# Kernel optimization log

Hardware: AMD Instinct MI355X
Metric: run time of the kernel (lower is better)

The kernel has to match this reference:

```python
import jax, jax.numpy as jnp
import numpy as np
from jax import lax

B, L = 128, 256
DW, DC = 100, 30
H = 400          # hidden_size (bidirectional total)
HD = H // 2      # per-direction hidden
NT = 18          # tag vocab size (BIOES)
VW, VC = 400000, 50000


def setup_inputs():
    key = jax.random.key(0)
    ks = iter(jax.random.split(key, 64))
    rn = lambda shape, s=0.1: jax.random.normal(next(ks), shape, jnp.float32) * s
    inp = {
        "words": jax.random.randint(next(ks), (B, L), 0, VW),
        "cap_words": jax.random.randint(next(ks), (B, L), 0, VC),
        "seq_len": jax.random.randint(next(ks), (B,), L // 2, L + 1),
        "target": jax.random.randint(next(ks), (B, L), 0, NT),
        "word_emb": rn((VW, DW)),
        "char_emb": rn((VC, DC)),
    }
    for l, din in ((0, DW + DC), (1, H)):
        for d in ("f", "b"):
            inp[f"W_ih_l{l}{d}"] = rn((4 * HD, din))
            inp[f"W_hh_l{l}{d}"] = rn((4 * HD, HD))
            inp[f"b_ih_l{l}{d}"] = rn((4 * HD,))
            inp[f"b_hh_l{l}{d}"] = rn((4 * HD,))
    inp["Wf"], inp["bf"] = rn((NT, HD)), jnp.zeros((NT,), jnp.float32)
    inp["Wb"], inp["bb"] = rn((NT, HD)), jnp.zeros((NT,), jnp.float32)
    inp["trans"] = rn((NT, NT))
    return inp


def _lstm_dir(x, W_ih, W_hh, b_ih, b_hh):
    # x: [B, L, D] -> hidden states [B, L, HD]; torch gate order i, f, g, o
    Bsz = x.shape[0]
    def step(carry, xt):
        h, c = carry
        g = xt @ W_ih.T + b_ih + h @ W_hh.T + b_hh
        i, f, gg, o = jnp.split(g, 4, axis=-1)
        c = jax.nn.sigmoid(f) * c + jax.nn.sigmoid(i) * jnp.tanh(gg)
        h = jax.nn.sigmoid(o) * jnp.tanh(c)
        return (h, c), h
    init = (jnp.zeros((Bsz, HD), x.dtype), jnp.zeros((Bsz, HD), x.dtype))
    _, hs = lax.scan(step, init, jnp.swapaxes(x, 0, 1))
    return jnp.swapaxes(hs, 0, 1)


def _rev(x, seq_len):
    # reverse each sequence within its true length (padding stays in place),
    # emulating pack_padded_sequence semantics for the backward direction
    t = jnp.arange(x.shape[1])[None, :]
    idx = jnp.where(t < seq_len[:, None], seq_len[:, None] - 1 - t, t)
    return jnp.take_along_axis(x, idx[:, :, None], axis=1)


def _crf_nll(logits, tags, mask, trans):
    # normalizer: forward algorithm, logsumexp scan over time with mask
    def step(alpha, inp):
        emit, m = inp  # emit: [B, NT], m: [B] bool
        new = jax.nn.logsumexp(alpha[:, :, None] + trans[None] + emit[:, None, :], axis=1)
        return jnp.where(m[:, None], new, alpha), None
    emits = jnp.swapaxes(logits, 0, 1)  # [L, B, NT]
    ms = jnp.swapaxes(mask, 0, 1)
    alpha, _ = lax.scan(step, emits[0], (emits[1:], ms[1:]))
    z = jax.nn.logsumexp(alpha, axis=1)
    # gold path score
    mf = mask.astype(logits.dtype)
    emit_sc = jnp.take_along_axis(logits, tags[:, :, None], axis=2)[:, :, 0]
    gold = jnp.sum(emit_sc * mf, axis=1) + jnp.sum(trans[tags[:, :-1], tags[:, 1:]] * mf[:, 1:], axis=1)
    return z - gold  # per-sample negative log-likelihood, shape [B]


def _model(words, cap_words, seq_len, target, word_emb, char_emb,
           W_ih_l0f, W_hh_l0f, b_ih_l0f, b_hh_l0f, W_ih_l0b, W_hh_l0b, b_ih_l0b, b_hh_l0b,
           W_ih_l1f, W_hh_l1f, b_ih_l1f, b_hh_l1f, W_ih_l1b, W_hh_l1b, b_ih_l1b, b_hh_l1b,
           Wf, bf, Wb, bb, trans):
    mask = jnp.arange(L)[None, :] < seq_len[:, None]  # [B, L] bool
    mf = mask.astype(jnp.float32)[:, :, None]
    x = jnp.concatenate([word_emb[words], char_emb[cap_words]], axis=-1)
    layers = (((W_ih_l0f, W_hh_l0f, b_ih_l0f, b_hh_l0f), (W_ih_l0b, W_hh_l0b, b_ih_l0b, b_hh_l0b)),
              ((W_ih_l1f, W_hh_l1f, b_ih_l1f, b_hh_l1f), (W_ih_l1b, W_hh_l1b, b_ih_l1b, b_hh_l1b)))
    h = x
    for fp, bp in layers:
        fwd = _lstm_dir(h, *fp)
        bwd = _rev(_lstm_dir(_rev(h, seq_len), *bp), seq_len)
        h = jnp.concatenate([fwd, bwd], axis=-1) * mf  # zero padded steps like packed LSTM
    forwards, backwards = h[..., :HD], h[..., HD:]
    logits = forwards @ Wf.T + bf + backwards @ Wb.T + bb
    return _crf_nll(logits, target, mask, trans)


def reference(words, cap_words, seq_len, target, word_emb, char_emb,
              W_ih_l0f, W_hh_l0f, b_ih_l0f, b_hh_l0f, W_ih_l0b, W_hh_l0b, b_ih_l0b, b_hh_l0b,
              W_ih_l1f, W_hh_l1f, b_ih_l1f, b_hh_l1f, W_ih_l1b, W_hh_l1b, b_ih_l1b, b_hh_l1b,
              Wf, bf, Wb, bb, trans):
    return _model(words, cap_words, seq_len, target, word_emb, char_emb,
                  W_ih_l0f, W_hh_l0f, b_ih_l0f, b_hh_l0f, W_ih_l0b, W_hh_l0b, b_ih_l0b, b_hh_l0b,
                  W_ih_l1f, W_hh_l1f, b_ih_l1f, b_hh_l1f, W_ih_l1b, W_hh_l1b, b_ih_l1b, b_hh_l1b,
                  Wf, bf, Wb, bb, trans)
```

## Files before the change

### kernel.cpp

```cpp
#include <hip/hip_runtime.h>
#include <math.h>

#define B_   128
#define L_   256
#define DW_  100
#define DC_  30
#define HD_  200
#define NT_  18
#define SG   4
#define KP0  160
#define KP1  416

typedef _Float16 half8 __attribute__((ext_vector_type(8)));
typedef _Float16 half4 __attribute__((ext_vector_type(4)));
typedef float    f32x4 __attribute__((ext_vector_type(4)));

__device__ __forceinline__ float frcp_(float x) { return __builtin_amdgcn_rcpf(x); }
__device__ __forceinline__ float sigm_(float x) { return frcp_(1.0f + __expf(-x)); }
__device__ __forceinline__ float tanh_(float x) { return 1.0f - 2.0f * frcp_(1.0f + __expf(2.0f * x)); }

__global__ void k_embed(const int* __restrict__ words, const int* __restrict__ caps,
                        const float* __restrict__ wemb, const float* __restrict__ cemb,
                        _Float16* __restrict__ x) {
    int pos = blockIdx.x;
    int w = words[pos], c = caps[pos];
    _Float16* xp = x + (size_t)pos * KP0;
    for (int t = threadIdx.x; t < KP0; t += blockDim.x) {
        float v = 0.f;
        if (t < DW_) v = wemb[(size_t)w * DW_ + t];
        else if (t < DW_ + DC_) v = cemb[(size_t)c * DC_ + (t - DW_)];
        xp[t] = (_Float16)v;
    }
}

__global__ void k_perm_ih16(const float* __restrict__ src, _Float16* __restrict__ dst,
                            int K, int Kpad, int colOff) {
    int i = blockIdx.x * blockDim.x + threadIdx.x;
    if (i >= 800 * Kpad) return;
    int r = i / Kpad, k = i - r * Kpad;
    int jh = r % 200, g = r / 200;
    int col = colOff + (jh << 2) + g;
    dst[(size_t)col * Kpad + k] = (k < K) ? (_Float16)src[(size_t)r * K + k] : (_Float16)0.f;
}

__global__ void k_bias_perm(const float* bi_f, const float* bh_f,
                            const float* bi_b, const float* bh_b, float* bias) {
    int j = blockIdx.x * blockDim.x + threadIdx.x;
    if (j >= 1600) return;
    int dir = j / 800, r = j - dir * 800;
    int col = dir * 800 + ((r % 200) << 2) + (r / 200);
    bias[col] = dir ? (bi_b[r] + bh_b[r]) : (bi_f[r] + bh_f[r]);
}

__global__ void k_wlog(const float* __restrict__ Wf, const float* __restrict__ bfv,
                       const float* __restrict__ Wb, const float* __restrict__ bbv,
                       float* __restrict__ wlog, float* __restrict__ blog) {
    int i = blockIdx.x * blockDim.x + threadIdx.x;
    if (i < NT_ * 400) {
        int t = i / 400, k = i - t * 400;
        wlog[i] = (k < HD_) ? Wf[t * HD_ + k] : Wb[t * HD_ + (k - HD_)];
    }
    if (i < NT_) blog[i] = bfv[i] + bbv[i];
}

__global__ __launch_bounds__(256) void k_gemm16(const _Float16* __restrict__ A,
                                                const _Float16* __restrict__ Bt,
                                                const float* __restrict__ bias,
                                                _Float16* __restrict__ C,
                                                int Kpad) {
    __shared__ __align__(16) _Float16 sA[128 * 40];
    __shared__ __align__(16) _Float16 sB[64 * 40];
    const int tid = threadIdx.x;
    const int w = tid >> 6, l = tid & 63, l15 = l & 15, lq = l >> 4;
    const int m0 = blockIdx.y * 128, n0 = blockIdx.x * 64;
    const int rw = (w >> 1) * 64, cw = (w & 1) * 32;
    f32x4 acc[4][2];
    #pragma unroll
    for (int i = 0; i < 4; i++)
        #pragma unroll
        for (int j = 0; j < 2; j++) acc[i][j] = f32x4{0.f, 0.f, 0.f, 0.f};

    for (int k0 = 0; k0 < Kpad; k0 += 32) {
        {
            int m = tid >> 1, c = (tid & 1) << 4;
            const _Float16* ap = A + (size_t)(m0 + m) * Kpad + k0 + c;
            *(half8*)&sA[m * 40 + c]     = *(const half8*)ap;
            *(half8*)&sA[m * 40 + c + 8] = *(const half8*)(ap + 8);
        }
        {
            int n = tid >> 2, k8 = (tid & 3) << 3;
            *(half8*)&sB[n * 40 + k8] = *(const half8*)&Bt[(size_t)(n0 + n) * Kpad + k0 + k8];
        }
        __syncthreads();
        half8 aF[4], bF[2];
        #pragma unroll
        for (int i = 0; i < 4; i++) aF[i] = *(const half8*)&sA[(rw + i * 16 + l15) * 40 + lq * 8];
        #pragma unroll
        for (int j = 0; j < 2; j++) bF[j] = *(const half8*)&sB[(cw + j * 16 + l15) * 40 + lq * 8];
        #pragma unroll
        for (int i = 0; i < 4; i++)
            #pragma unroll
            for (int j = 0; j < 2; j++)
                acc[i][j] = __builtin_amdgcn_mfma_f32_16x16x32_f16(aF[i], bF[j], acc[i][j], 0, 0, 0);
        __syncthreads();
    }
    #pragma unroll
    for (int j = 0; j < 2; j++) {
        int n = n0 + cw + j * 16 + l15;
        float bv = bias[n];
        #pragma unroll
        for (int i = 0; i < 4; i++) {
            int mrow = m0 + rw + i * 16 + lq * 4;
            #pragma unroll
            for (int r = 0; r < 4; r++)
                C[(size_t)(mrow + r) * 1600 + n] = (_Float16)(acc[i][j][r] + bv);
        }
    }
}

__global__ __launch_bounds__(512, 2) void k_scan4(const _Float16* __restrict__ gates,
                                                  const float* __restrict__ Whh_f,
                                                  const float* __restrict__ Whh_b,
                                                  const int* __restrict__ seq_len,
                                                  _Float16* __restrict__ hout, int ldH) {
    const int dir = blockIdx.x & 1;
    const int b0  = (blockIdx.x >> 1) * SG;
    const int tid = threadIdx.x;
    const int w   = tid >> 6;
    const int l   = tid & 63;
    const int l15 = l & 15;
    const int lq  = l >> 4;

    __shared__ __align__(16) _Float16 hA[2][16 * 232];
    __shared__ __align__(16) float    gbw[8 * 476];
    __shared__ __align__(16) _Float16 bEx[2 * 7 * 512];
    __shared__ __align__(16) _Float16 glds[2][3200];
    __shared__ int ssl[SG];

    const float* W = dir ? Whh_b : Whh_f;
    const int nT = (w < 2) ? 7 : 6;

    half8 Breg[6][7];
    #pragma unroll
    for (int i = 0; i < 6; i++) {
        int n  = (w * 6 + i) * 16 + l15;
        int jh = n >> 2, g = n & 3;
        const float* Wr = W + (size_t)(g * 200 + jh) * 200;
        #pragma unroll
        for (int kt = 0; kt < 7; kt++) {
            int k0 = kt * 32 + lq * 8;
            half8 f;
            #pragma unroll
            for (int j = 0; j < 8; j++) {
                int k = k0 + j;
                f[j] = (k < 200) ? (_Float16)Wr[k] : (_Float16)0.f;
            }
            Breg[i][kt] = f;
        }
    }
    if (w < 2) {
        int n  = (48 + w) * 16 + l15;
        int jh = n >> 2, g = n & 3;
        const float* Wr = W + (size_t)(g * 200 + jh) * 200;
        for (int kt = 0; kt < 7; kt++) {
            int k0 = kt * 32 + lq * 8;
            half8 f;
            for (int j = 0; j < 8; j++) {
                int k = k0 + j;
                f[j] = (k < 200) ? (_Float16)Wr[k] : (_Float16)0.f;
            }
            *(half8*)&bEx[(w * 7 + kt) * 512 + l * 8] = f;
        }
    }
    for (int i = tid; i < 2 * 16 * 232; i += 512) (&hA[0][0])[i] = (_Float16)0.f;
    if (tid < SG) ssl[tid] = seq_len[b0 + tid];

    const int  v    = tid;
    const bool stv  = v < 400;
    const int  m_st = v / 100;
    const int  u_st = v - m_st * 100;
    const int  sl_st = stv ? seq_len[b0 + m_st] : L_;
    const _Float16* gbase_st = gates + ((size_t)(b0 + m_st) * L_) * 1600 + dir * 800 + u_st * 8;

    const int cA = l;
    const int cB = l + 64;
    const bool vB = cB < nT * 16;
    const int iA = cA >> 4,           nhA = (cA >> 2) & 3, mA = cA & 3;
    const int iB = cB >> 4,           nhB = (cB >> 2) & 3, mB = cB & 3;
    const int igA = (iA < 6) ? (w * 6 + iA) : (48 + w);
    const int igB = (iB < 6) ? (w * 6 + iB) : (48 + w);
    const int hAcol = igA * 4 + nhA;
    const int hBcol = igB * 4 + nhB;
    float csA = 0.f, csB = 0.f;

    half8 stg;
    if (stv) {
        int rn = dir ? ((sl_st > 0) ? sl_st - 1 : 0) : 0;
        stg = *(const half8*)(gbase_st + (size_t)rn * 1600);
        *(half8*)&glds[0][v * 8] = stg;
    }
    __syncthreads();

    const f32x4 Cz = {0.f, 0.f, 0.f, 0.f};
    for (int t = 0; t < L_; t++) {
        const int p = t & 1;

        half8 stgn;
        const bool doStg = stv && (t + 1 < L_);
        if (doStg) {
            int tn = t + 1;
            int rn = dir ? ((tn < sl_st) ? sl_st - 1 - tn : tn) : tn;
            stgn = *(const half8*)(gbase_st + (size_t)rn * 1600);
        }

        if (t > 0) {
            int tp = t - 1;
            #pragma unroll
            for (int kk = 0; kk < 2; kk++) {
                int idx = tid + (kk << 9);
                if (idx < 800) {
                    int b = (idx * 5243) >> 20;
                    int hh = idx - b * 200;
                    int slb = ssl[b];
                    int row = dir ? ((tp < slb) ? slb - 1 - tp : tp) : tp;
                    _Float16 val = (tp < slb) ? hA[p][b * 232 + hh] : (_Float16)0.f;
                    hout[((size_t)(b0 + b) * L_ + row) * ldH + dir * HD_ + hh] = val;
                }
            }
        }

        f32x4 C[7];
        #pragma unroll
        for (int i = 0; i < 7; i++) C[i] = Cz;
        #pragma unroll
        for (int kt = 0; kt < 7; kt++) {
            half8 aF = *(const half8*)&hA[p][l15 * 232 + kt * 32 + lq * 8];
            #pragma unroll
            for (int i = 0; i < 6; i++)
                C[i] = __builtin_amdgcn_mfma_f32_16x16x32_f16(aF, Breg[i][kt], C[i], 0, 0, 0);
            if (w < 2) {
                half8 bF = *(const half8*)&bEx[(w * 7 + kt) * 512 + l * 8];
                C[6] = __builtin_amdgcn_mfma_f32_16x16x32_f16(aF, bF, C[6], 0, 0, 0);
            }
        }
        if (l < 16) {
            #pragma unroll
            for (int i = 0; i < 7; i++) if (i < nT) {
                #pragma unroll
                for (int r = 0; r < 4; r++)
                    gbw[w * 476 + i * 68 + r * 17 + l15] = C[i][r];
            }
        }

        {
            const float* gw = &gbw[w * 476 + iA * 68 + mA * 17 + nhA * 4];
            half4 gi4 = *(const half4*)&glds[p][mA * 800 + 4 * hAcol];
            float xi = gw[0] + (float)gi4[0];
            float xf = gw[1] + (float)gi4[1];
            float xg = gw[2] + (float)gi4[2];
            float xo = gw[3] + (float)gi4[3];
            float cn = sigm_(xf) * csA + sigm_(xi) * tanh_(xg);
            csA = cn;
            hA[1 - p][mA * 232 + hAcol] = (_Float16)(sigm_(xo) * tanh_(cn));
        }
        if (vB) {
            const float* gw = &gbw[w * 476 + iB * 68 + mB * 17 + nhB * 4];
            half4 gi4 = *(const half4*)&glds[p][mB * 800 + 4 * hBcol];
            float xi = gw[0] + (float)gi4[0];
            float xf = gw[1] + (float)gi4[1];
            float xg = gw[2] + (float)gi4[2];
            float xo = gw[3] + (float)gi4[3];
            float cn = sigm_(xf) * csB + sigm_(xi) * tanh_(xg);
            csB = cn;
            hA[1 - p][mB * 232 + hBcol] = (_Float16)(sigm_(xo) * tanh_(cn));
        }

        if (doStg) *(half8*)&glds[1 - p][v * 8] = stgn;

        __syncthreads();
    }
    {
        int tp = L_ - 1;
        #pragma unroll
        for (int kk = 0; kk < 2; kk++) {
            int idx = tid + (kk << 9);
            if (idx < 800) {
                int b = (idx * 5243) >> 20;
                int hh = idx - b * 200;
                int slb = ssl[b];
                int row = dir ? ((tp < slb) ? slb - 1 - tp : tp) : tp;
                _Float16 val = (tp < slb) ? hA[0][b * 232 + hh] : (_Float16)0.f;
                hout[((size_t)(b0 + b) * L_ + row) * ldH + dir * HD_ + hh] = val;
            }
        }
    }
}

__global__ __launch_bounds__(256) void k_logits(const _Float16* __restrict__ h1,
                                                const float* __restrict__ wlog,
                                                const float* __restrict__ blog,
                                                float* __restrict__ logits) {
    __shared__ float sh[8][400];
    __shared__ float sw[NT_ * 400];
    int p0 = blockIdx.x * 8;
    for (int i = threadIdx.x; i < 8 * 400; i += 256)
        sh[i / 400][i % 400] = (float)h1[(size_t)p0 * 400 + i];
    for (int i = threadIdx.x; i < NT_ * 400; i += 256) sw[i] = wlog[i];
    __syncthreads();
    if (threadIdx.x < 8 * NT_) {
        int pi = threadIdx.x / NT_, tg = threadIdx.x % NT_;
        float a = blog[tg];
        #pragma unroll 4
        for (int k = 0; k < 400; k++) a += sh[pi][k] * sw[tg * 400 + k];
        logits[((size_t)(p0 + pi)) * NT_ + tg] = a;
    }
}

__global__ __launch_bounds__(64) void k_crf(const float* __restrict__ logits,
                                            const int* __restrict__ target,
                                            const int* __restrict__ seq_len,
                                            const float* __restrict__ trans,
                                            float* __restrict__ out) {
    int b = blockIdx.x, tid = threadIdx.x;
    __shared__ float str[NT_ * NT_];
    __shared__ float alpha[NT_];
    __shared__ float sgold[1];
    for (int i = tid; i < NT_ * NT_; i += 64) str[i] = trans[i];
    int sl = seq_len[b];
    const float* lg = logits + (size_t)b * L_ * NT_;
    const int* tg = target + (size_t)b * L_;
    if (tid < NT_) alpha[tid] = lg[tid];
    float gacc = 0.f;
    for (int t = tid; t < L_; t += 64) {
        if (t < sl) {
            gacc += lg[t * NT_ + tg[t]];
            if (t >= 1) gacc += trans[tg[t - 1] * NT_ + tg[t]];
        }
    }
    #pragma unroll
    for (int off = 32; off; off >>= 1) gacc += __shfl_down(gacc, off);
    if (tid == 0) sgold[0] = gacc;
    __syncthreads();
    for (int t = 1; t < L_; t++) {
        if (t < sl) {
            float v = 0.f;
            if (tid < NT_) {
                float mx = -1e30f;
                #pragma unroll
                for (int i = 0; i < NT_; i++) mx = fmaxf(mx, alpha[i] + str[i * NT_ + tid]);
                float s = 0.f;
                #pragma unroll
                for (int i = 0; i < NT_; i++) s += __expf(alpha[i] + str[i * NT_ + tid] - mx);
                v = mx + __logf(s) + lg[t * NT_ + tid];
            }
            __syncthreads();
            if (tid < NT_) alpha[tid] = v;
            __syncthreads();
        }
    }
    if (tid == 0) {
        float mx = -1e30f;
        for (int i = 0; i < NT_; i++) mx = fmaxf(mx, alpha[i]);
        float s = 0.f;
        for (int i = 0; i < NT_; i++) s += __expf(alpha[i] - mx);
        out[b] = (mx + __logf(s)) - sgold[0];
    }
}

extern "C" void kernel_launch(void* const* d_in, const int* in_sizes, int n_in,
                              void* d_out, int out_size, void* d_ws, size_t ws_size,
                              hipStream_t stream) {
    const int*   words  = (const int*)d_in[0];
    const int*   caps   = (const int*)d_in[1];
    const int*   seq    = (const int*)d_in[2];
    const int*   target = (const int*)d_in[3];
    const float* wemb   = (const float*)d_in[4];
    const float* cemb   = (const float*)d_in[5];
    const float* Wih0f  = (const float*)d_in[6];
    const float* Whh0f  = (const float*)d_in[7];
    const float* bih0f  = (const float*)d_in[8];
    const float* bhh0f  = (const float*)d_in[9];
    const float* Wih0b  = (const float*)d_in[10];
    const float* Whh0b  = (const float*)d_in[11];
    const float* bih0b  = (const float*)d_in[12];
    const float* bhh0b  = (const float*)d_in[13];
    const float* Wih1f  = (const float*)d_in[14];
    const float* Whh1f  = (const float*)d_in[15];
    const float* bih1f  = (const float*)d_in[16];
    const float* bhh1f  = (const float*)d_in[17];
    const float* Wih1b  = (const float*)d_in[18];
    const float* Whh1b  = (const float*)d_in[19];
    const float* bih1b  = (const float*)d_in[20];
    const float* bhh1b  = (const float*)d_in[21];
    const float* Wf     = (const float*)d_in[22];
    const float* bfv    = (const float*)d_in[23];
    const float* Wb     = (const float*)d_in[24];
    const float* bbv    = (const float*)d_in[25];
    const float* trans  = (const float*)d_in[26];

    char* base = (char*)d_ws;
    _Float16* gatesH = (_Float16*)(base + 0);
    _Float16* xbuf   = (_Float16*)(base + 104857600);
    _Float16* h0b    = (_Float16*)(base + 115343360);
    _Float16* h1b    = xbuf;
    float* logitsb   = (float*)(base + 142606336);
    _Float16* wihT0  = (_Float16*)(base + 144965632);
    _Float16* wihT1  = (_Float16*)(base + 145477632);
    float* bias0     = (float*)(base + 146808832);
    float* bias1     = (float*)(base + 146815232);
    float* wlog      = (float*)(base + 146821632);
    float* blog      = (float*)(base + 146850432);

    k_perm_ih16<<<(800 * KP0 + 255) / 256, 256, 0, stream>>>(Wih0f, wihT0, 130, KP0, 0);
    k_perm_ih16<<<(800 * KP0 + 255) / 256, 256, 0, stream>>>(Wih0b, wihT0, 130, KP0, 800);
    k_perm_ih16<<<(800 * KP1 + 255) / 256, 256, 0, stream>>>(Wih1f, wihT1, 400, KP1, 0);
    k_perm_ih16<<<(800 * KP1 + 255) / 256, 256, 0, stream>>>(Wih1b, wihT1, 400, KP1, 800);
    k_bias_perm<<<7, 256, 0, stream>>>(bih0f, bhh0f, bih0b, bhh0b, bias0);
    k_bias_perm<<<7, 256, 0, stream>>>(bih1f, bhh1f, bih1b, bhh1b, bias1);
    k_wlog<<<(NT_ * 400 + 255) / 256, 256, 0, stream>>>(Wf, bfv, Wb, bbv, wlog, blog);

    k_embed<<<B_ * L_, 128, 0, stream>>>(words, caps, wemb, cemb, xbuf);

    hipMemsetAsync(h0b, 0, (size_t)32768 * KP1 * sizeof(_Float16), stream);

    k_gemm16<<<dim3(25, 256), 256, 0, stream>>>(xbuf, wihT0, bias0, gatesH, KP0);
    k_scan4<<<(B_ / SG) * 2, 512, 0, stream>>>(gatesH, Whh0f, Whh0b, seq, h0b, KP1);

    k_gemm16<<<dim3(25, 256), 256, 0, stream>>>(h0b, wihT1, bias1, gatesH, KP1);
    k_scan4<<<(B_ / SG) * 2, 512, 0, stream>>>(gatesH, Whh1f, Whh1b, seq, h1b, 400);

    k_logits<<<(B_ * L_) / 8, 256, 0, stream>>>(h1b, wlog, blog, logitsb);
    k_crf<<<B_, 64, 0, stream>>>(logitsb, target, seq, trans, (float*)d_out);
}
```

Before: 1.482 ms.

## Swap MFMA operands so gate results land in registers, drop LDS gate staging

The recurrent MFMA now puts the weights as the A operand and hidden state as B, so each lane's accumulator holds the four gates (i,f,g,o) of one hidden unit for one batch row. The cell update then runs directly from registers on the 4 active lanes per 16, removing the gbw LDS round trip that was written and reread every timestep. The hidden-state output store is also narrowed to one 32-bit store per thread instead of two scalar fp16 stores. In exchange only a quarter of the lanes do the nonlinear math, serially over up to 7 tiles, and more cell-state registers are held per lane.

```diff
diff --git a/kernel.cpp b/kernel.cpp
--- a/kernel.cpp
+++ b/kernel.cpp
@@ -118,7 +118,7 @@
     }
 }
 
-__global__ __launch_bounds__(512, 2) void k_scan4(const _Float16* __restrict__ gates,
+__global__ __launch_bounds__(512, 2) void k_scan5(const _Float16* __restrict__ gates,
                                                   const float* __restrict__ Whh_f,
                                                   const float* __restrict__ Whh_b,
                                                   const int* __restrict__ seq_len,
@@ -132,7 +132,6 @@
     const int lq  = l >> 4;
 
     __shared__ __align__(16) _Float16 hA[2][16 * 232];
-    __shared__ __align__(16) float    gbw[8 * 476];
     __shared__ __align__(16) _Float16 bEx[2 * 7 * 512];
     __shared__ __align__(16) _Float16 glds[2][3200];
     __shared__ int ssl[SG];
@@ -182,21 +181,21 @@
     const int  sl_st = stv ? seq_len[b0 + m_st] : L_;
     const _Float16* gbase_st = gates + ((size_t)(b0 + m_st) * L_) * 1600 + dir * 800 + u_st * 8;
 
-    const int cA = l;
-    const int cB = l + 64;
-    const bool vB = cB < nT * 16;
-    const int iA = cA >> 4,           nhA = (cA >> 2) & 3, mA = cA & 3;
-    const int iB = cB >> 4,           nhB = (cB >> 2) & 3, mB = cB & 3;
-    const int igA = (iA < 6) ? (w * 6 + iA) : (48 + w);
-    const int igB = (iB < 6) ? (w * 6 + iB) : (48 + w);
-    const int hAcol = igA * 4 + nhA;
-    const int hBcol = igB * 4 + nhB;
-    float csA = 0.f, csB = 0.f;
-
-    half8 stg;
+    const bool act = (l15 < 4);
+    const int  m   = l15;
+    int hcol[7];
+    #pragma unroll
+    for (int i = 0; i < 7; i++) {
+        int tile = (i < 6) ? (w * 6 + i) : (48 + w);
+        hcol[i] = tile * 4 + lq;
+    }
+    float cs[7];
+    #pragma unroll
+    for (int i = 0; i < 7; i++) cs[i] = 0.f;
+
     if (stv) {
         int rn = dir ? ((sl_st > 0) ? sl_st - 1 : 0) : 0;
-        stg = *(const half8*)(gbase_st + (size_t)rn * 1600);
+        half8 stg = *(const half8*)(gbase_st + (size_t)rn * 1600);
         *(half8*)&glds[0][v * 8] = stg;
     }
     __syncthreads();
@@ -213,20 +212,14 @@
             stgn = *(const half8*)(gbase_st + (size_t)rn * 1600);
         }
 
-        if (t > 0) {
+        if (t > 0 && stv) {
             int tp = t - 1;
-            #pragma unroll
-            for (int kk = 0; kk < 2; kk++) {
-                int idx = tid + (kk << 9);
-                if (idx < 800) {
-                    int b = (idx * 5243) >> 20;
-                    int hh = idx - b * 200;
-                    int slb = ssl[b];
-                    int row = dir ? ((tp < slb) ? slb - 1 - tp : tp) : tp;
-                    _Float16 val = (tp < slb) ? hA[p][b * 232 + hh] : (_Float16)0.f;
-                    hout[((size_t)(b0 + b) * L_ + row) * ldH + dir * HD_ + hh] = val;
-                }
-            }
+            int b  = m_st;
+            int hp = u_st;
+            int slb = ssl[b];
+            int row = dir ? ((tp < slb) ? slb - 1 - tp : tp) : tp;
+            unsigned int val = (tp < slb) ? *(const unsigned int*)&hA[p][b * 232 + 2 * hp] : 0u;
+            *(unsigned int*)&hout[((size_t)(b0 + b) * L_ + row) * ldH + dir * HD_ + 2 * hp] = val;
         }
 
         f32x4 C[7];
@@ -234,65 +227,42 @@
         for (int i = 0; i < 7; i++) C[i] = Cz;
         #pragma unroll
         for (int kt = 0; kt < 7; kt++) {
-            half8 aF = *(const half8*)&hA[p][l15 * 232 + kt * 32 + lq * 8];
+            half8 hF = *(const half8*)&hA[p][l15 * 232 + kt * 32 + lq * 8];
             #pragma unroll
             for (int i = 0; i < 6; i++)
-                C[i] = __builtin_amdgcn_mfma_f32_16x16x32_f16(aF, Breg[i][kt], C[i], 0, 0, 0);
+                C[i] = __builtin_amdgcn_mfma_f32_16x16x32_f16(Breg[i][kt], hF, C[i], 0, 0, 0);
             if (w < 2) {
                 half8 bF = *(const half8*)&bEx[(w * 7 + kt) * 512 + l * 8];
-                C[6] = __builtin_amdgcn_mfma_f32_16x16x32_f16(aF, bF, C[6], 0, 0, 0);
+                C[6] = __builtin_amdgcn_mfma_f32_16x16x32_f16(bF, hF, C[6], 0, 0, 0);
             }
         }
-        if (l < 16) {
+
+        if (act) {
             #pragma unroll
             for (int i = 0; i < 7; i++) if (i < nT) {
-                #pragma unroll
-                for (int r = 0; r < 4; r++)
-                    gbw[w * 476 + i * 68 + r * 17 + l15] = C[i][r];
+                half4 gi4 = *(const half4*)&glds[p][m * 800 + 4 * hcol[i]];
+                float xi = C[i][0] + (float)gi4[0];
+                float xf = C[i][1] + (float)gi4[1];
+                float xg = C[i][2] + (float)gi4[2];
+                float xo = C[i][3] + (float)gi4[3];
+                float cn = sigm_(xf) * cs[i] + sigm_(xi) * tanh_(xg);
+                cs[i] = cn;
+                hA[1 - p][m * 232 + hcol[i]] = (_Float16)(sigm_(xo) * tanh_(cn));
             }
         }
 
-        {
-            const float* gw = &gbw[w * 476 + iA * 68 + mA * 17 + nhA * 4];
-            half4 gi4 = *(const half4*)&glds[p][mA * 800 + 4 * hAcol];
-            float xi = gw[0] + (float)gi4[0];
-            float xf = gw[1] + (float)gi4[1];
-            float xg = gw[2] + (float)gi4[2];
-            float xo = gw[3] + (float)gi4[3];
-            float cn = sigm_(xf) * csA + sigm_(xi) * tanh_(xg);
-            csA = cn;
-            hA[1 - p][mA * 232 + hAcol] = (_Float16)(sigm_(xo) * tanh_(cn));
-        }
-        if (vB) {
-            const float* gw = &gbw[w * 476 + iB * 68 + mB * 17 + nhB * 4];
-            half4 gi4 = *(const half4*)&glds[p][mB * 800 + 4 * hBcol];
-            float xi = gw[0] + (float)gi4[0];
-            float xf = gw[1] + (float)gi4[1];
-            float xg = gw[2] + (float)gi4[2];
-            float xo = gw[3] + (float)gi4[3];
-            float cn = sigm_(xf) * csB + sigm_(xi) * tanh_(xg);
-            csB = cn;
-            hA[1 - p][mB * 232 + hBcol] = (_Float16)(sigm_(xo) * tanh_(cn));
-        }
-
         if (doStg) *(half8*)&glds[1 - p][v * 8] = stgn;
 
         __syncthreads();
     }
-    {
+    if (stv) {
         int tp = L_ - 1;
-        #pragma unroll
-        for (int kk = 0; kk < 2; kk++) {
-            int idx = tid + (kk << 9);
-            if (idx < 800) {
-                int b = (idx * 5243) >> 20;
-                int hh = idx - b * 200;
-                int slb = ssl[b];
-                int row = dir ? ((tp < slb) ? slb - 1 - tp : tp) : tp;
-                _Float16 val = (tp < slb) ? hA[0][b * 232 + hh] : (_Float16)0.f;
-                hout[((size_t)(b0 + b) * L_ + row) * ldH + dir * HD_ + hh] = val;
-            }
-        }
+        int b  = m_st;
+        int hp = u_st;
+        int slb = ssl[b];
+        int row = dir ? ((tp < slb) ? slb - 1 - tp : tp) : tp;
+        unsigned int val = (tp < slb) ? *(const unsigned int*)&hA[0][b * 232 + 2 * hp] : 0u;
+        *(unsigned int*)&hout[((size_t)(b0 + b) * L_ + row) * ldH + dir * HD_ + 2 * hp] = val;
     }
 }
 
@@ -424,10 +394,10 @@
     hipMemsetAsync(h0b, 0, (size_t)32768 * KP1 * sizeof(_Float16), stream);
 
     k_gemm16<<<dim3(25, 256), 256, 0, stream>>>(xbuf, wihT0, bias0, gatesH, KP0);
-    k_scan4<<<(B_ / SG) * 2, 512, 0, stream>>>(gatesH, Whh0f, Whh0b, seq, h0b, KP1);
+    k_scan5<<<(B_ / SG) * 2, 512, 0, stream>>>(gatesH, Whh0f, Whh0b, seq, h0b, KP1);
 
     k_gemm16<<<dim3(25, 256), 256, 0, stream>>>(h0b, wihT1, bias1, gatesH, KP1);
-    k_scan4<<<(B_ / SG) * 2, 512, 0, stream>>>(gatesH, Whh1f, Whh1b, seq, h1b, 400);
+    k_scan5<<<(B_ / SG) * 2, 512, 0, stream>>>(gatesH, Whh1f, Whh1b, seq, h1b, 400);
 
     k_logits<<<(B_ * L_) / 8, 256, 0, stream>>>(h1b, wlog, blog, logitsb);
     k_crf<<<B_, 64, 0, stream>>>(logitsb, target, seq, trans, (float*)d_out);
```

New measurement: 1.753 ms. 18.2% more time.
